# Kernel optimization log

Hardware: AMD Instinct MI355X
Metric: run time of the kernel (lower is better)

The kernel has to match this reference:

```python
import jax, jax.numpy as jnp
import numpy as np

EPS = 1e-12  # F.normalize default eps


def setup_inputs() -> dict:
    key = jax.random.key(0)
    k1, k2, k3 = jax.random.split(key, 3)
    B, C, H, W = 4, 64, 64, 64
    background = jax.random.normal(k1, (B, C, H, W), dtype=jnp.float32)
    foreground = jax.random.normal(k2, (B, C, H, W), dtype=jnp.float32)
    # binary mask, broadcast over channels
    mask = jnp.round(jax.random.uniform(k3, (B, 1, H, W), dtype=jnp.float32))
    return {"background": background, "foreground": foreground, "mask": mask}


def _l2norm(x, axis):
    # matches torch F.normalize: x / max(||x||, eps)
    n = jnp.sqrt(jnp.sum(x * x, axis=axis, keepdims=True))
    return x / jnp.maximum(n, EPS)


def reference(background, foreground, mask):
    B, C, H, W = background.shape
    bg_flat = background.reshape(B, C, H * W)   # [B, C, K]
    fg_flat = foreground.reshape(B, C, H * W)   # [B, C, Q]
    norm_bg = _l2norm(bg_flat, axis=1)
    norm_fg = _l2norm(fg_flat, axis=1)
    # cosine-similarity scores [B, K, Q]
    attention = jnp.einsum('bck,bcq->bkq', norm_bg, norm_fg)
    attention = jax.nn.softmax(attention, axis=1)  # over bg (key) axis
    attended = jnp.einsum('bck,bkq->bcq', bg_flat, attention)
    attended = attended.reshape(B, C, H, W)
    return foreground * (1.0 - mask) + attended * mask
```

## Files before the change

kernel.cpp:

```cpp
#include <hip/hip_runtime.h>
#include <math.h>

#define CC 64
#define HWN 4096
#define QB 64
#define KSPLIT 8
#define KT 32
#define NITER (HWN / KSPLIT / KT)
#define NKC (HWN / KT)

typedef __attribute__((ext_vector_type(8))) short bf16x8;
typedef __attribute__((ext_vector_type(4))) short bf16x4;
typedef __attribute__((ext_vector_type(4))) float f32x4;

__device__ __align__(16) unsigned short g_bgT[4][HWN][CC];
__device__ __align__(16) unsigned short g_bgN[4][NKC][CC][KT];
__device__ __align__(16) unsigned short g_fgT[4][HWN][CC];

static __device__ __forceinline__ unsigned int f2bf(float x) {
  union { float f; unsigned int u; } v; v.f = x;
  return (v.u + 0x7fffu + ((v.u >> 16) & 1u)) >> 16;
}
static __device__ __forceinline__ unsigned int packbf(float lo, float hi) {
  return f2bf(lo) | (f2bf(hi) << 16);
}

__global__ __launch_bounds__(256) void prep_kernel(const float* __restrict__ bg,
                                                   const float* __restrict__ fg) {
  __shared__ float lds[64 * 65];
  const int bid = blockIdx.x;
  const int kt = bid & 63, b = (bid >> 6) & 3, which = bid >> 8;
  const float* src = (which ? fg : bg) + (size_t)b * CC * HWN + kt * 64;
  const int tid = threadIdx.x;

  {
    int c = tid >> 2, k0 = (tid & 3) * 16;
#pragma unroll
    for (int j4 = 0; j4 < 4; ++j4) {
      float4 v = *(const float4*)(src + (size_t)c * HWN + k0 + 4 * j4);
      lds[(k0 + 4 * j4 + 0) * 65 + c] = v.x;
      lds[(k0 + 4 * j4 + 1) * 65 + c] = v.y;
      lds[(k0 + 4 * j4 + 2) * 65 + c] = v.z;
      lds[(k0 + 4 * j4 + 3) * 65 + c] = v.w;
    }
  }
  __syncthreads();

  const int k = tid >> 2, u = tid & 3;
  float ss = 0.f;
#pragma unroll
  for (int j = 0; j < 16; ++j) {
    float v = lds[k * 65 + u * 16 + j];
    ss = fmaf(v, v, ss);
  }
  ss += __shfl_xor(ss, 1, 64);
  ss += __shfl_xor(ss, 2, 64);
  const float s = 1.0f / fmaxf(sqrtf(ss), 1e-12f);

  {
    unsigned int* gT32 = (unsigned int*)(which ? &g_fgT[0][0][0] : &g_bgT[0][0][0]);
    size_t R = (size_t)b * HWN + kt * 64 + k;
    unsigned int w8[8];
#pragma unroll
    for (int i = 0; i < 8; ++i) {
      int c2 = u * 16 + 2 * i;
      w8[i] = packbf(lds[k * 65 + c2] * s, lds[k * 65 + c2 + 1] * s);
    }
    *(uint4*)&gT32[R * 32 + u * 8]     = make_uint4(w8[0], w8[1], w8[2], w8[3]);
    *(uint4*)&gT32[R * 32 + u * 8 + 4] = make_uint4(w8[4], w8[5], w8[6], w8[7]);
  }

  if (which == 0) {
    unsigned int* gN32 = (unsigned int*)&g_bgN[0][0][0][0];
    int cN = tid >> 2, vN = tid & 3;
    unsigned int n8[8];
#pragma unroll
    for (int i = 0; i < 8; ++i) {
      int kk = vN * 16 + 2 * i;
      n8[i] = packbf(lds[kk * 65 + cN], lds[(kk + 1) * 65 + cN]);
    }
    int kc = kt * 2 + (vN >> 1);
    size_t RN = (((size_t)b * NKC + kc) * CC + cN) * (KT / 2) + (vN & 1) * 8;
    *(uint4*)&gN32[RN]     = make_uint4(n8[0], n8[1], n8[2], n8[3]);
    *(uint4*)&gN32[RN + 4] = make_uint4(n8[4], n8[5], n8[6], n8[7]);
  }
}

#define ML_OFF 69632
#define SMEM_BYTES 71680
__global__ __launch_bounds__(512, 2) void attn_kernel(const float* __restrict__ fg,
                                                      const float* __restrict__ mask,
                                                      float* __restrict__ out) {
  __shared__ __align__(16) char smem[SMEM_BYTES];
  const int wg = blockIdx.x;
  const int wgp = (wg & 7) * 32 + (wg >> 3);
  const int b = wgp >> 6;
  const int q0 = (wgp & 63) * QB;
  const int tid = threadIdx.x;
  const int lane = tid & 63;
  const int ks = tid >> 6;
  const int m16 = lane & 15;
  const int quad = lane >> 4;

  bf16x8 Bf[4][2];
#pragma unroll
  for (int qf = 0; qf < 4; ++qf)
#pragma unroll
    for (int h = 0; h < 2; ++h)
      Bf[qf][h] = *(const bf16x8*)&g_fgT[b][q0 + qf * 16 + m16][h * 32 + quad * 8];

  const unsigned short* const baseT = &g_bgT[b][ks * 512][0];
  const unsigned short* const baseN = &g_bgN[b][ks * 16][0][0];

  float* mL = (float*)(smem + ML_OFF);

  float l_run[4] = {0.f, 0.f, 0.f, 0.f};
  f32x4 O[4][4];
#pragma unroll
  for (int t = 0; t < 4; ++t)
#pragma unroll
    for (int qf = 0; qf < 4; ++qf) O[t][qf] = (f32x4){0.f, 0.f, 0.f, 0.f};

  auto loadT = [&](bf16x8 (&T)[2][2], int ch) {
#pragma unroll
    for (int i = 0; i < 2; ++i)
#pragma unroll
      for (int h = 0; h < 2; ++h)
        T[i][h] = *(const bf16x8*)(baseT + (size_t)(ch * 32 + i * 16 + m16) * CC +
                                   h * 32 + quad * 8);
  };
  auto loadA = [&](bf16x4 (&A)[4][2], int ch) {
#pragma unroll
    for (int ct = 0; ct < 4; ++ct)
#pragma unroll
      for (int i = 0; i < 2; ++i)
        A[ct][i] = *(const bf16x4*)(baseN + (size_t)ch * (CC * KT) +
                                    (ct * 16 + m16) * KT + i * 16 + quad * 4);
  };

  bf16x8 Ta[2][2], Tb[2][2];
  bf16x4 Aa[4][2], Ab[4][2];

  auto iter = [&](int it, bf16x8 (&T)[2][2], bf16x4 (&A)[4][2],
                  bf16x8 (&Tn)[2][2], bf16x4 (&An)[4][2]) {
    if (it + 1 < NITER) {
      loadT(Tn, it + 1);
      loadA(An, it + 1);
      asm volatile("s_waitcnt vmcnt(12)" ::: "memory");
    } else {
      asm volatile("s_waitcnt vmcnt(0)" ::: "memory");
    }

    f32x4 S[4][2];
    __builtin_amdgcn_s_setprio(1);
#pragma unroll
    for (int i = 0; i < 2; ++i)
#pragma unroll
      for (int qf = 0; qf < 4; ++qf) {
        f32x4 acc = {0.f, 0.f, 0.f, 0.f};
        acc = __builtin_amdgcn_mfma_f32_16x16x32_bf16(T[i][0], Bf[qf][0], acc, 0, 0, 0);
        acc = __builtin_amdgcn_mfma_f32_16x16x32_bf16(T[i][1], Bf[qf][1], acc, 0, 0, 0);
        S[qf][i] = acc;
      }
    __builtin_amdgcn_s_setprio(0);

    bf16x4 Pp[4][2];
#pragma unroll
    for (int qf = 0; qf < 4; ++qf)
#pragma unroll
      for (int i = 0; i < 2; ++i) {
        float pe[4];
#pragma unroll
        for (int r = 0; r < 4; ++r) {
          pe[r] = __expf(S[qf][i][r] - 1.0f);
          l_run[qf] += pe[r];
        }
        union { float f; unsigned int u; } x0, x1, x2, x3;
        x0.f = pe[0]; x1.f = pe[1]; x2.f = pe[2]; x3.f = pe[3];
        union { unsigned int u[2]; bf16x4 v; } pk;
        pk.u[0] = __builtin_amdgcn_perm(x1.u + 0x8000u, x0.u + 0x8000u, 0x07060302u);
        pk.u[1] = __builtin_amdgcn_perm(x3.u + 0x8000u, x2.u + 0x8000u, 0x07060302u);
        Pp[qf][i] = pk.v;
      }

    __builtin_amdgcn_s_setprio(1);
#pragma unroll
    for (int ct = 0; ct < 4; ++ct)
#pragma unroll
      for (int qf = 0; qf < 4; ++qf) {
        O[ct][qf] = __builtin_amdgcn_mfma_f32_16x16x16bf16_1k(A[ct][0], Pp[qf][0],
                                                              O[ct][qf], 0, 0, 0);
        O[ct][qf] = __builtin_amdgcn_mfma_f32_16x16x16bf16_1k(A[ct][1], Pp[qf][1],
                                                              O[ct][qf], 0, 0, 0);
      }
    __builtin_amdgcn_s_setprio(0);
  };

  loadT(Ta, 0);
  loadA(Aa, 0);

  for (int it2 = 0; it2 < NITER; it2 += 2) {
    iter(it2,     Ta, Aa, Tb, Ab);
    iter(it2 + 1, Tb, Ab, Ta, Aa);
  }

#pragma unroll
  for (int qf = 0; qf < 4; ++qf) {
    l_run[qf] += __shfl_xor(l_run[qf], 16, 64);
    l_run[qf] += __shfl_xor(l_run[qf], 32, 64);
  }
  if (quad == 0) {
#pragma unroll
    for (int qf = 0; qf < 4; ++qf) mL[ks * 64 + qf * 16 + m16] = l_run[qf];
  }
  float* mO = (float*)smem;
  const float* fgB = fg + (size_t)b * CC * HWN;
  const float* mk = mask + (size_t)b * HWN;
  float* outB = out + (size_t)b * CC * HWN;

#pragma unroll
  for (int half = 0; half < 2; ++half) {
    __syncthreads();
#pragma unroll
    for (int qh = 0; qh < 2; ++qh) {
      int qf = half * 2 + qh;
#pragma unroll
      for (int t = 0; t < 4; ++t)
#pragma unroll
        for (int r = 0; r < 4; ++r)
          mO[(ks * 64 + 16 * t + quad * 4 + r) * 34 + qh * 16 + m16] = O[t][qf][r];
    }
    __syncthreads();
    {
      int q = tid & 31, cb = tid >> 5;
      int qglob = q0 + half * 32 + q;
      float L = 0.f;
#pragma unroll
      for (int s = 0; s < 8; ++s) L += mL[s * 64 + half * 32 + q];
      float invL = 1.0f / L;
      float mv = mk[qglob];
#pragma unroll
      for (int e = 0; e < 4; ++e) {
        int c = cb * 4 + e;
        float acc = 0.f;
#pragma unroll
        for (int s = 0; s < 8; ++s) acc += mO[(s * 64 + c) * 34 + q];
        float att = acc * invL;
        float fgv = fgB[(size_t)c * HWN + qglob];
        outB[(size_t)c * HWN + qglob] = fgv + mv * (att - fgv);
      }
    }
  }
}

extern "C" void kernel_launch(void* const* d_in, const int* in_sizes, int n_in,
                              void* d_out, int out_size, void* d_ws, size_t ws_size,
                              hipStream_t stream) {
  const float* background = (const float*)d_in[0];
  const float* foreground = (const float*)d_in[1];
  const float* mask       = (const float*)d_in[2];
  float* out = (float*)d_out;
  prep_kernel<<<512, 256, 0, stream>>>(background, foreground);
  attn_kernel<<<dim3(HWN / QB * 4), 512, 0, stream>>>(foreground, mask, out);
}
```

Baseline: 101.3 us.

## Split query tile across wave pairs with 1024-thread blocks and single-buffered prefetch

Doubles the block to 1024 threads so each of the 8 key-split slices is handled by two waves, each covering 32 of the 64 queries. This halves per-wave accumulators and fragments. The double-buffered register prefetch is replaced by single buffers: the next T chunk is loaded after the score MFMAs and the next A chunk after the PV MFMAs. The aim is to cut register pressure and add waves for latency hiding, at the cost of duplicated bg loads per block and less prefetch distance.

Result: slower. 128.7 us (+27.1%).

```diff
diff --git a/kernel.cpp b/kernel.cpp
--- a/kernel.cpp
+++ b/kernel.cpp
@@ -88,9 +88,9 @@
 
 #define ML_OFF 69632
 #define SMEM_BYTES 71680
-__global__ __launch_bounds__(512, 2) void attn_kernel(const float* __restrict__ fg,
-                                                      const float* __restrict__ mask,
-                                                      float* __restrict__ out) {
+__global__ __launch_bounds__(1024) void attn_kernel(const float* __restrict__ fg,
+                                                    const float* __restrict__ mask,
+                                                    float* __restrict__ out) {
   __shared__ __align__(16) char smem[SMEM_BYTES];
   const int wg = blockIdx.x;
   const int wgp = (wg & 7) * 32 + (wg >> 3);
@@ -98,30 +98,35 @@
   const int q0 = (wgp & 63) * QB;
   const int tid = threadIdx.x;
   const int lane = tid & 63;
-  const int ks = tid >> 6;
+  const int w = tid >> 6;
+  const int qg = w & 1;
+  const int ks = w >> 1;
   const int m16 = lane & 15;
   const int quad = lane >> 4;
 
-  bf16x8 Bf[4][2];
-#pragma unroll
-  for (int qf = 0; qf < 4; ++qf)
+  bf16x8 Bf[2][2];
+#pragma unroll
+  for (int qf = 0; qf < 2; ++qf)
 #pragma unroll
     for (int h = 0; h < 2; ++h)
-      Bf[qf][h] = *(const bf16x8*)&g_fgT[b][q0 + qf * 16 + m16][h * 32 + quad * 8];
+      Bf[qf][h] = *(const bf16x8*)&g_fgT[b][q0 + qg * 32 + qf * 16 + m16][h * 32 + quad * 8];
 
   const unsigned short* const baseT = &g_bgT[b][ks * 512][0];
   const unsigned short* const baseN = &g_bgN[b][ks * 16][0][0];
 
   float* mL = (float*)(smem + ML_OFF);
 
-  float l_run[4] = {0.f, 0.f, 0.f, 0.f};
-  f32x4 O[4][4];
+  float l_run[2] = {0.f, 0.f};
+  f32x4 O[4][2];
 #pragma unroll
   for (int t = 0; t < 4; ++t)
 #pragma unroll
-    for (int qf = 0; qf < 4; ++qf) O[t][qf] = (f32x4){0.f, 0.f, 0.f, 0.f};
-
-  auto loadT = [&](bf16x8 (&T)[2][2], int ch) {
+    for (int qf = 0; qf < 2; ++qf) O[t][qf] = (f32x4){0.f, 0.f, 0.f, 0.f};
+
+  bf16x8 T[2][2];
+  bf16x4 A[4][2];
+
+  auto loadT = [&](int ch) {
 #pragma unroll
     for (int i = 0; i < 2; ++i)
 #pragma unroll
@@ -129,7 +134,7 @@
         T[i][h] = *(const bf16x8*)(baseT + (size_t)(ch * 32 + i * 16 + m16) * CC +
                                    h * 32 + quad * 8);
   };
-  auto loadA = [&](bf16x4 (&A)[4][2], int ch) {
+  auto loadA = [&](int ch) {
 #pragma unroll
     for (int ct = 0; ct < 4; ++ct)
 #pragma unroll
@@ -138,25 +143,18 @@
                                     (ct * 16 + m16) * KT + i * 16 + quad * 4);
   };
 
-  bf16x8 Ta[2][2], Tb[2][2];
-  bf16x4 Aa[4][2], Ab[4][2];
-
-  auto iter = [&](int it, bf16x8 (&T)[2][2], bf16x4 (&A)[4][2],
-                  bf16x8 (&Tn)[2][2], bf16x4 (&An)[4][2]) {
-    if (it + 1 < NITER) {
-      loadT(Tn, it + 1);
-      loadA(An, it + 1);
-      asm volatile("s_waitcnt vmcnt(12)" ::: "memory");
-    } else {
-      asm volatile("s_waitcnt vmcnt(0)" ::: "memory");
-    }
-
-    f32x4 S[4][2];
+  loadT(0);
+  loadA(0);
+
+  for (int it = 0; it < NITER; ++it) {
+    asm volatile("s_waitcnt vmcnt(8)" ::: "memory");
+
+    f32x4 S[2][2];
     __builtin_amdgcn_s_setprio(1);
 #pragma unroll
     for (int i = 0; i < 2; ++i)
 #pragma unroll
-      for (int qf = 0; qf < 4; ++qf) {
+      for (int qf = 0; qf < 2; ++qf) {
         f32x4 acc = {0.f, 0.f, 0.f, 0.f};
         acc = __builtin_amdgcn_mfma_f32_16x16x32_bf16(T[i][0], Bf[qf][0], acc, 0, 0, 0);
         acc = __builtin_amdgcn_mfma_f32_16x16x32_bf16(T[i][1], Bf[qf][1], acc, 0, 0, 0);
@@ -164,9 +162,11 @@
       }
     __builtin_amdgcn_s_setprio(0);
 
-    bf16x4 Pp[4][2];
-#pragma unroll
-    for (int qf = 0; qf < 4; ++qf)
+    if (it + 1 < NITER) loadT(it + 1);
+
+    bf16x4 Pp[2][2];
+#pragma unroll
+    for (int qf = 0; qf < 2; ++qf)
 #pragma unroll
       for (int i = 0; i < 2; ++i) {
         float pe[4];
@@ -183,35 +183,35 @@
         Pp[qf][i] = pk.v;
       }
 
+    if (it + 1 < NITER) {
+      asm volatile("s_waitcnt vmcnt(4)" ::: "memory");
+    } else {
+      asm volatile("s_waitcnt vmcnt(0)" ::: "memory");
+    }
+
     __builtin_amdgcn_s_setprio(1);
 #pragma unroll
     for (int ct = 0; ct < 4; ++ct)
 #pragma unroll
-      for (int qf = 0; qf < 4; ++qf) {
+      for (int qf = 0; qf < 2; ++qf) {
         O[ct][qf] = __builtin_amdgcn_mfma_f32_16x16x16bf16_1k(A[ct][0], Pp[qf][0],
                                                               O[ct][qf], 0, 0, 0);
         O[ct][qf] = __builtin_amdgcn_mfma_f32_16x16x16bf16_1k(A[ct][1], Pp[qf][1],
                                                               O[ct][qf], 0, 0, 0);
       }
     __builtin_amdgcn_s_setprio(0);
-  };
-
-  loadT(Ta, 0);
-  loadA(Aa, 0);
-
-  for (int it2 = 0; it2 < NITER; it2 += 2) {
-    iter(it2,     Ta, Aa, Tb, Ab);
-    iter(it2 + 1, Tb, Ab, Ta, Aa);
-  }
-
-#pragma unroll
-  for (int qf = 0; qf < 4; ++qf) {
+
+    if (it + 1 < NITER) loadA(it + 1);
+  }
+
+#pragma unroll
+  for (int qf = 0; qf < 2; ++qf) {
     l_run[qf] += __shfl_xor(l_run[qf], 16, 64);
     l_run[qf] += __shfl_xor(l_run[qf], 32, 64);
   }
   if (quad == 0) {
 #pragma unroll
-    for (int qf = 0; qf < 4; ++qf) mL[ks * 64 + qf * 16 + m16] = l_run[qf];
+    for (int qf = 0; qf < 2; ++qf) mL[ks * 64 + qg * 32 + qf * 16 + m16] = l_run[qf];
   }
   float* mO = (float*)smem;
   const float* fgB = fg + (size_t)b * CC * HWN;
@@ -221,14 +221,14 @@
 #pragma unroll
   for (int half = 0; half < 2; ++half) {
     __syncthreads();
-#pragma unroll
-    for (int qh = 0; qh < 2; ++qh) {
-      int qf = half * 2 + qh;
-#pragma unroll
-      for (int t = 0; t < 4; ++t)
-#pragma unroll
-        for (int r = 0; r < 4; ++r)
-          mO[(ks * 64 + 16 * t + quad * 4 + r) * 34 + qh * 16 + m16] = O[t][qf][r];
+    if (qg == half) {
+#pragma unroll
+      for (int qf = 0; qf < 2; ++qf)
+#pragma unroll
+        for (int t = 0; t < 4; ++t)
+#pragma unroll
+          for (int r = 0; r < 4; ++r)
+            mO[(ks * 64 + 16 * t + quad * 4 + r) * 34 + qf * 16 + m16] = O[t][qf][r];
     }
     __syncthreads();
     {
@@ -240,8 +240,8 @@
       float invL = 1.0f / L;
       float mv = mk[qglob];
 #pragma unroll
-      for (int e = 0; e < 4; ++e) {
-        int c = cb * 4 + e;
+      for (int e = 0; e < 2; ++e) {
+        int c = cb * 2 + e;
         float acc = 0.f;
 #pragma unroll
         for (int s = 0; s < 8; ++s) acc += mO[(s * 64 + c) * 34 + q];
@@ -261,5 +261,5 @@
   const float* mask       = (const float*)d_in[2];
   float* out = (float*)d_out;
   prep_kernel<<<512, 256, 0, stream>>>(background, foreground);
-  attn_kernel<<<dim3(HWN / QB * 4), 512, 0, stream>>>(foreground, mask, out);
-}
+  attn_kernel<<<dim3(HWN / QB * 4), 1024, 0, stream>>>(foreground, mask, out);
+}
```
